# Performance work log

Hardware: AMD Instinct MI355X
Metric: run time of the kernel (lower is better)

The kernel has to match this reference:

```python
import math
import jax, jax.numpy as jnp
import numpy as np

B, S, D, H = 4, 2048, 768, 12
HD = D // H  # 64


def setup_inputs() -> dict:
    key = jax.random.key(0)
    ks = jax.random.split(key, 10)
    sc = 0.02
    return {
        "hidden_states": jax.random.normal(ks[0], (B, S, D), dtype=jnp.float32),
        "attention_mask": jax.random.randint(ks[1], (1, H, S, S), 0, 2).astype(jnp.bool_),
        "q_w": jax.random.normal(ks[2], (D, D), dtype=jnp.float32) * sc,
        "q_b": jax.random.normal(ks[3], (D,), dtype=jnp.float32) * sc,
        "k_w": jax.random.normal(ks[4], (D, D), dtype=jnp.float32) * sc,
        "k_b": jax.random.normal(ks[5], (D,), dtype=jnp.float32) * sc,
        "v_w": jax.random.normal(ks[6], (D, D), dtype=jnp.float32) * sc,
        "v_b": jax.random.normal(ks[7], (D,), dtype=jnp.float32) * sc,
        "out_w": jax.random.normal(ks[8], (D, D), dtype=jnp.float32) * sc,
        "out_b": jax.random.normal(ks[9], (D,), dtype=jnp.float32) * sc,
    }


def _split_heads(x):
    # [B, S, D] -> [B, H, S, HD]
    b, s, _ = x.shape
    return x.reshape(b, s, H, HD).transpose(0, 2, 1, 3)


def reference(hidden_states, attention_mask, q_w, q_b, k_w, k_b, v_w, v_b, out_w, out_b):
    q = _split_heads(hidden_states @ q_w.T + q_b)
    k = _split_heads(hidden_states @ k_w.T + k_b)
    v = _split_heads(hidden_states @ v_w.T + v_b)
    scores = jnp.einsum("bhqd,bhkd->bhqk", q, k) / math.sqrt(HD)
    # prune_mode, before softmax: masked_fill(~mask, -inf)
    scores = jnp.where(attention_mask, scores, -jnp.inf)
    probs = jax.nn.softmax(scores, axis=-1)  # [B, H, S, S]
    ctx = jnp.einsum("bhqk,bhkd->bhqd", probs, v)
    ctx = ctx.transpose(0, 2, 1, 3).reshape(hidden_states.shape[0], -1, D)
    return ctx @ out_w.T + out_b
```

## Files before the change

kernel.cpp:

```cpp
#include <hip/hip_runtime.h>
#include <hip/hip_bf16.h>

#define B_ 4
#define S_ 2048
#define D_ 768
#define H_ 12
#define HD_ 64

typedef __attribute__((ext_vector_type(8))) short bf16x8;
typedef __attribute__((ext_vector_type(4))) float floatx4;

#define QSCALE 0.18033688011112042f

__device__ __forceinline__ unsigned short f2bf(float x) {
    union { float f; unsigned int u; } v; v.f = x;
    unsigned int r = v.u + 0x7fffu + ((v.u >> 16) & 1u);
    return (unsigned short)(r >> 16);
}

__device__ __forceinline__ unsigned int pk2bf(float a, float b) {
    __hip_bfloat162 h = __float22bfloat162_rn(make_float2(a, b));
    unsigned int u;
    __builtin_memcpy(&u, &h, 4);
    return u;
}

__device__ __forceinline__ void gload_lds16(const void* g, void* l) {
    __builtin_amdgcn_global_load_lds(
        (const __attribute__((address_space(1))) unsigned int*)g,
        (__attribute__((address_space(3))) unsigned int*)l, 16, 0, 0);
}

__device__ __forceinline__ bf16x8 ld_b64x2(const unsigned short* p) {
    union { bf16x8 v; unsigned long long q[2]; } u;
    u.q[0] = *(const unsigned long long*)p;
    u.q[1] = *(const unsigned long long*)(p + 4);
    return u.v;
}

__global__ void cast_f32_bf16(const float* __restrict__ src,
                              unsigned short* __restrict__ dst, int n4) {
    int i = blockIdx.x * 256 + threadIdx.x;
    if (i >= n4) return;
    float4 f = ((const float4*)src)[i];
    ushort4 o;
    o.x = f2bf(f.x); o.y = f2bf(f.y); o.z = f2bf(f.z); o.w = f2bf(f.w);
    ((ushort4*)dst)[i] = o;
}

__global__ void cast_w4(const float* __restrict__ w0, const float* __restrict__ w1,
                        const float* __restrict__ w2, const float* __restrict__ w3,
                        unsigned short* __restrict__ dst, int n4 ) {
    const float* src = (blockIdx.y == 0) ? w0 : (blockIdx.y == 1) ? w1
                     : (blockIdx.y == 2) ? w2 : w3;
    unsigned short* d = dst + (size_t)blockIdx.y * (size_t)n4 * 4;
    int i = blockIdx.x * 256 + threadIdx.x;
    if (i >= n4) return;
    float4 f = ((const float4*)src)[i];
    ushort4 o;
    o.x = f2bf(f.x); o.y = f2bf(f.y); o.z = f2bf(f.z); o.w = f2bf(f.w);
    ((ushort4*)d)[i] = o;
}

__global__ void pack_mask(const int* __restrict__ mask,
                          unsigned long long* __restrict__ bits) {
    size_t gw = (size_t)(blockIdx.x * 256 + threadIdx.x) >> 6;
    int lane = threadIdx.x & 63;
    size_t base = gw * 256;
    unsigned long long b0 = __ballot(mask[base + lane] != 0);
    unsigned long long b1 = __ballot(mask[base + 64 + lane] != 0);
    unsigned long long b2 = __ballot(mask[base + 128 + lane] != 0);
    unsigned long long b3 = __ballot(mask[base + 192 + lane] != 0);
    if (lane == 0) {
        bits[gw * 4 + 0] = b0; bits[gw * 4 + 1] = b1;
        bits[gw * 4 + 2] = b2; bits[gw * 4 + 3] = b3;
    }
}

__global__ __launch_bounds__(256) void qkv_gemm(
    const unsigned short* __restrict__ Xb,
    const unsigned short* __restrict__ Wq, const unsigned short* __restrict__ Wk,
    const unsigned short* __restrict__ Wv,
    const float* __restrict__ bq, const float* __restrict__ bk,
    const float* __restrict__ bv,
    unsigned short* __restrict__ Qo, unsigned short* __restrict__ Ko,
    unsigned short* __restrict__ Vo)
{
    const int z = blockIdx.z;
    const unsigned short* W = (z == 0) ? Wq : (z == 1) ? Wk : Wv;
    const float* bias = (z == 0) ? bq : (z == 1) ? bk : bv;
    unsigned short* Out = (z == 0) ? Qo : (z == 1) ? Ko : Vo;
    const float scale = (z == 0) ? QSCALE : 1.0f;

    const int m0 = blockIdx.x * 128;
    const int n0 = blockIdx.y * 128;

    __shared__ alignas(16) unsigned short SM[8192];
    unsigned short* As = SM;
    unsigned short* Bs = SM + 4096;

    const int t = threadIdx.x;
    const int lane = t & 63, w = t >> 6;
    const int c = lane & 15, quad = lane >> 4;
    const int wm = (w & 1) * 64, wn = (w >> 1) * 64;

    floatx4 acc[4][4];
#pragma unroll
    for (int i = 0; i < 4; i++)
#pragma unroll
        for (int j = 0; j < 4; j++) acc[i][j] = (floatx4){0.f, 0.f, 0.f, 0.f};

    for (int k0 = 0; k0 < 768; k0 += 32) {
#pragma unroll
        for (int i = 0; i < 2; i++) {
            int chunk = i * 4 + w;
            int row = chunk * 16 + (lane >> 2);
            int c8 = (lane & 3) * 8;
            gload_lds16(&Xb[(size_t)(m0 + row) * 768 + k0 + c8], &As[chunk * 512]);
            gload_lds16(&W [(size_t)(n0 + row) * 768 + k0 + c8], &Bs[chunk * 512]);
        }
        __syncthreads();
        bf16x8 a[4], b[4];
#pragma unroll
        for (int i = 0; i < 4; i++)
            a[i] = *(const bf16x8*)&As[(wm + i * 16 + c) * 32 + quad * 8];
#pragma unroll
        for (int j = 0; j < 4; j++)
            b[j] = *(const bf16x8*)&Bs[(wn + j * 16 + c) * 32 + quad * 8];
#pragma unroll
        for (int i = 0; i < 4; i++)
#pragma unroll
            for (int j = 0; j < 4; j++)
                acc[i][j] = __builtin_amdgcn_mfma_f32_16x16x32_bf16(
                    a[i], b[j], acc[i][j], 0, 0, 0);
        __syncthreads();
    }

    if (z == 2) {
        const int bb = m0 >> 11, ssb = m0 & 2047;
#pragma unroll
        for (int half = 0; half < 2; half++) {
            if ((w >> 1) == half) {
#pragma unroll
                for (int j = 0; j < 4; j++) {
                    int n_l = j * 16 + c;
                    float bias_n = bias[n0 + half * 64 + n_l];
#pragma unroll
                    for (int i = 0; i < 4; i++) {
#pragma unroll
                        for (int r = 0; r < 4; r++) {
                            int m = wm + i * 16 + quad * 4 + r;
                            int ms = m ^ (c << 3);
                            SM[n_l * 128 + ms] = f2bf(acc[i][j][r] + bias_n);
                        }
                    }
                }
            }
            __syncthreads();
#pragma unroll
            for (int rb = 0; rb < 2; rb++) {
                int n_l = (t >> 3) + rb * 32;
                int ch = t & 7;
                int n_abs = n0 + half * 64 + n_l;
                int hh = n_abs >> 6, dd = n_abs & 63;
                unsigned short* dst =
                    Out + (((size_t)(bb * H_ + hh)) * 64 + dd) * S_ + ssb;
#pragma unroll
                for (int p = 0; p < 2; p++) {
                    int mc = ch + p * 8;
                    uint4 v = *(const uint4*)&SM[n_l * 128 + ((mc ^ (n_l & 15)) * 8)];
                    *(uint4*)&dst[mc * 8] = v;
                }
            }
            __syncthreads();
        }
    } else {
#pragma unroll
        for (int i = 0; i < 4; i++) {
#pragma unroll
            for (int j = 0; j < 4; j++) {
                int nn = n0 + wn + j * 16 + c;
                float bias_n = bias[nn];
                int hh = nn >> 6, dd = nn & 63;
#pragma unroll
                for (int r = 0; r < 4; r++) {
                    int mm = m0 + wm + i * 16 + quad * 4 + r;
                    int bb = mm >> 11, ss = mm & 2047;
                    float v = (acc[i][j][r] + bias_n) * scale;
                    Out[(((size_t)(bb * H_ + hh)) * S_ + ss) * 64 + dd] = f2bf(v);
                }
            }
        }
    }
}

__global__ __launch_bounds__(256) void out_gemm(
    const unsigned short* __restrict__ Cb, const unsigned short* __restrict__ Wo,
    const float* __restrict__ bo, float* __restrict__ out)
{
    const int m0 = blockIdx.x * 128;
    const int n0 = blockIdx.y * 128;

    __shared__ alignas(16) unsigned short As[128 * 32];
    __shared__ alignas(16) unsigned short Bs[128 * 32];

    const int t = threadIdx.x;
    const int lane = t & 63, w = t >> 6;
    const int c = lane & 15, quad = lane >> 4;
    const int wm = (w & 1) * 64, wn = (w >> 1) * 64;

    floatx4 acc[4][4];
#pragma unroll
    for (int i = 0; i < 4; i++)
#pragma unroll
        for (int j = 0; j < 4; j++) acc[i][j] = (floatx4){0.f, 0.f, 0.f, 0.f};

    for (int k0 = 0; k0 < 768; k0 += 32) {
#pragma unroll
        for (int i = 0; i < 2; i++) {
            int chunk = i * 4 + w;
            int row = chunk * 16 + (lane >> 2);
            int c8 = (lane & 3) * 8;
            gload_lds16(&Cb[(size_t)(m0 + row) * 768 + k0 + c8], &As[chunk * 512]);
            gload_lds16(&Wo[(size_t)(n0 + row) * 768 + k0 + c8], &Bs[chunk * 512]);
        }
        __syncthreads();
        bf16x8 a[4], b[4];
#pragma unroll
        for (int i = 0; i < 4; i++)
            a[i] = *(const bf16x8*)&As[(wm + i * 16 + c) * 32 + quad * 8];
#pragma unroll
        for (int j = 0; j < 4; j++)
            b[j] = *(const bf16x8*)&Bs[(wn + j * 16 + c) * 32 + quad * 8];
#pragma unroll
        for (int i = 0; i < 4; i++)
#pragma unroll
            for (int j = 0; j < 4; j++)
                acc[i][j] = __builtin_amdgcn_mfma_f32_16x16x32_bf16(
                    a[i], b[j], acc[i][j], 0, 0, 0);
        __syncthreads();
    }

#pragma unroll
    for (int i = 0; i < 4; i++) {
#pragma unroll
        for (int j = 0; j < 4; j++) {
            int nn = n0 + wn + j * 16 + c;
            float bias_n = bo[nn];
#pragma unroll
            for (int r = 0; r < 4; r++) {
                int mm = m0 + wm + i * 16 + quad * 4 + r;
                out[(size_t)mm * 768 + nn] = acc[i][j][r] + bias_n;
            }
        }
    }
}

__global__ __launch_bounds__(256) void attn(
    const unsigned short* __restrict__ Q, const unsigned short* __restrict__ K,
    const unsigned short* __restrict__ Vt,
    const unsigned long long* __restrict__ mbits,
    unsigned short* __restrict__ ctx)
{
    const int qt = blockIdx.x;
    const int bh = blockIdx.y;
    const int b = bh / H_, h = bh % H_;

    const unsigned short* Qp = Q + (size_t)bh * S_ * 64 + (size_t)qt * 64 * 64;
    const unsigned short* Kp = K + (size_t)bh * S_ * 64;
    const unsigned short* Vp = Vt + (size_t)bh * 64 * S_;

    __shared__ alignas(16) unsigned short Ks[2][64 * 64];
    __shared__ alignas(16) unsigned short Vs[2][64 * 64];
    __shared__ alignas(16) unsigned short Ps[4][16 * 68];

    const int t = threadIdx.x;
    const int lane = t & 63, w = t >> 6;
    const int c = lane & 15, quad = lane >> 4;

    bf16x8 aq0 = *(const bf16x8*)&Qp[(size_t)(w * 16 + c) * 64 + quad * 8];
    bf16x8 aq1 = *(const bf16x8*)&Qp[(size_t)(w * 16 + c) * 64 + 32 + quad * 8];

    const unsigned long long* mrow =
        mbits + ((size_t)h * S_ + qt * 64 + w * 16 + quad * 4) * (S_ / 64);

    floatx4 acc_o[4];
#pragma unroll
    for (int i = 0; i < 4; i++) acc_o[i] = (floatx4){0.f, 0.f, 0.f, 0.f};
    float lp[4] = {0.f, 0.f, 0.f, 0.f};

    const int srow = (lane >> 3);
    const int rc0 = ((quad     ) ^ (c & 7)) * 8;
    const int rc1 = ((quad + 4) ^ (c & 7)) * 8;

#pragma unroll
    for (int i = 0; i < 2; i++) {
        int chunk = i * 4 + w;
        int row = chunk * 8 + srow;
        int col8 = (((lane & 7) ^ ((row >> 2) & 7))) * 8;
        gload_lds16(&Kp[(size_t)row * 64 + col8], &Ks[0][chunk * 512]);
        gload_lds16(&Vp[(size_t)row * S_ + col8], &Vs[0][chunk * 512]);
    }

    for (int kt = 0; kt < S_ / 64; kt++) {
        const int cur = kt & 1;
        __syncthreads();
        if (kt + 1 < S_ / 64) {
#pragma unroll
            for (int i = 0; i < 2; i++) {
                int chunk = i * 4 + w;
                int row = chunk * 8 + srow;
                int col8 = (((lane & 7) ^ ((row >> 2) & 7))) * 8;
                gload_lds16(&Kp[(size_t)((kt + 1) * 64 + row) * 64 + col8],
                            &Ks[cur ^ 1][chunk * 512]);
                gload_lds16(&Vp[(size_t)row * S_ + (kt + 1) * 64 + col8],
                            &Vs[cur ^ 1][chunk * 512]);
            }
        }

        floatx4 sacc[4];
#pragma unroll
        for (int nt = 0; nt < 4; nt++) {
            int kr = 4 * c + nt;
            bf16x8 bk0 = *(const bf16x8*)&Ks[cur][kr * 64 + rc0];
            bf16x8 bk1 = *(const bf16x8*)&Ks[cur][kr * 64 + rc1];
            floatx4 zz = (floatx4){0.f, 0.f, 0.f, 0.f};
            zz = __builtin_amdgcn_mfma_f32_16x16x32_bf16(aq0, bk0, zz, 0, 0, 0);
            zz = __builtin_amdgcn_mfma_f32_16x16x32_bf16(aq1, bk1, zz, 0, 0, 0);
            sacc[nt] = zz;
        }

#pragma unroll
        for (int r = 0; r < 4; r++) {
            unsigned int nib = (unsigned int)(mrow[r * (S_ / 64) + kt] >> (4 * c)) & 15u;
            float p0 = (nib & 1u) ? __builtin_amdgcn_exp2f(sacc[0][r]) : 0.f;
            float p1 = (nib & 2u) ? __builtin_amdgcn_exp2f(sacc[1][r]) : 0.f;
            float p2 = (nib & 4u) ? __builtin_amdgcn_exp2f(sacc[2][r]) : 0.f;
            float p3 = (nib & 8u) ? __builtin_amdgcn_exp2f(sacc[3][r]) : 0.f;
            lp[r] += (p0 + p1) + (p2 + p3);
            unsigned long long pk =
                (unsigned long long)pk2bf(p0, p1) |
                ((unsigned long long)pk2bf(p2, p3) << 32);
            *(unsigned long long*)&Ps[w][(quad * 4 + r) * 68 + 4 * c] = pk;
        }
        asm volatile("" ::: "memory");

        bf16x8 ap0 = ld_b64x2(&Ps[w][c * 68 + quad * 8]);
        bf16x8 ap1 = ld_b64x2(&Ps[w][c * 68 + 32 + quad * 8]);
#pragma unroll
        for (int nt = 0; nt < 4; nt++) {
            int vr = 4 * c + nt;
            bf16x8 bv0 = *(const bf16x8*)&Vs[cur][vr * 64 + rc0];
            bf16x8 bv1 = *(const bf16x8*)&Vs[cur][vr * 64 + rc1];
            acc_o[nt] = __builtin_amdgcn_mfma_f32_16x16x32_bf16(ap0, bv0, acc_o[nt], 0, 0, 0);
            acc_o[nt] = __builtin_amdgcn_mfma_f32_16x16x32_bf16(ap1, bv1, acc_o[nt], 0, 0, 0);
        }
    }

#pragma unroll
    for (int r = 0; r < 4; r++) {
        float s = lp[r];
#pragma unroll
        for (int o = 1; o < 16; o <<= 1) s += __shfl_xor(s, o, 64);
        lp[r] = s;
    }

#pragma unroll
    for (int nt = 0; nt < 4; nt++) {
#pragma unroll
        for (int r = 0; r < 4; r++) {
            int qrow = qt * 64 + w * 16 + quad * 4 + r;
            int dd = 4 * c + nt;
            float v = acc_o[nt][r] / lp[r];
            ctx[((size_t)b * S_ + qrow) * 768 + h * 64 + dd] = f2bf(v);
        }
    }
}

extern "C" void kernel_launch(void* const* d_in, const int* in_sizes, int n_in,
                              void* d_out, int out_size, void* d_ws, size_t ws_size,
                              hipStream_t stream) {
    const float* hs    = (const float*)d_in[0];
    const int*   mask  = (const int*)d_in[1];
    const float* q_w   = (const float*)d_in[2];
    const float* q_b   = (const float*)d_in[3];
    const float* k_w   = (const float*)d_in[4];
    const float* k_b   = (const float*)d_in[5];
    const float* v_w   = (const float*)d_in[6];
    const float* v_b   = (const float*)d_in[7];
    const float* out_w = (const float*)d_in[8];
    const float* out_b = (const float*)d_in[9];
    float* out = (float*)d_out;

    unsigned short* Xb  = (unsigned short*)d_ws;
    unsigned short* Wqb = Xb + 6291456;
    unsigned short* Wkb = Wqb + 589824;
    unsigned short* Wvb = Wkb + 589824;
    unsigned short* Wob = Wvb + 589824;
    unsigned short* Qb  = Wob + 589824;
    unsigned short* Kb  = Qb + 6291456;
    unsigned short* Vtb = Kb + 6291456;
    unsigned short* Cb  = Vtb + 6291456;
    unsigned long long* mbits = (unsigned long long*)(Cb + 6291456);

    cast_f32_bf16<<<6144, 256, 0, stream>>>(hs, Xb, 1572864);
    cast_w4<<<dim3(576, 4), 256, 0, stream>>>(q_w, k_w, v_w, out_w, Wqb, 147456);
    pack_mask<<<49152, 256, 0, stream>>>(mask, mbits);
    qkv_gemm<<<dim3(64, 6, 3), 256, 0, stream>>>(Xb, Wqb, Wkb, Wvb,
                                                 q_b, k_b, v_b, Qb, Kb, Vtb);
    attn<<<dim3(32, 48), 256, 0, stream>>>(Qb, Kb, Vtb, mbits, Cb);
    out_gemm<<<dim3(64, 6), 256, 0, stream>>>(Cb, Wob, out_b, out);
}
```

Measured before the change: 508.1 us.

## Double attention query tile per block and stage GEMM epilogues through LDS

The attention kernel now processes 128 query rows per block, with each wave handling two 16-row subtiles. Each K/V tile loaded into shared memory is therefore reused across twice as many queries, halving K/V global traffic and the grid size. The Q/K epilogue of the QKV GEMM and the output GEMM epilogue now stage results through swizzled shared memory so global stores are coalesced 16-byte writes instead of scattered 2- or 4-byte ones. The trade-offs are fewer blocks (768), higher register pressure in attention, and extra barriers in the epilogues.

```diff
diff --git a/kernel.cpp b/kernel.cpp
--- a/kernel.cpp
+++ b/kernel.cpp
@@ -136,8 +136,8 @@
         __syncthreads();
     }
 
+    const int bb = m0 >> 11, ssb = m0 & 2047;
     if (z == 2) {
-        const int bb = m0 >> 11, ssb = m0 & 2047;
 #pragma unroll
         for (int half = 0; half < 2; half++) {
             if ((w >> 1) == half) {
@@ -176,20 +176,37 @@
         }
     } else {
 #pragma unroll
-        for (int i = 0; i < 4; i++) {
-#pragma unroll
-            for (int j = 0; j < 4; j++) {
-                int nn = n0 + wn + j * 16 + c;
-                float bias_n = bias[nn];
-                int hh = nn >> 6, dd = nn & 63;
-#pragma unroll
-                for (int r = 0; r < 4; r++) {
-                    int mm = m0 + wm + i * 16 + quad * 4 + r;
-                    int bb = mm >> 11, ss = mm & 2047;
-                    float v = (acc[i][j][r] + bias_n) * scale;
-                    Out[(((size_t)(bb * H_ + hh)) * S_ + ss) * 64 + dd] = f2bf(v);
+        for (int half = 0; half < 2; half++) {
+            if ((w >> 1) == half) {
+#pragma unroll
+                for (int j = 0; j < 4; j++) {
+                    float bias_n = bias[n0 + half * 64 + j * 16 + c];
+#pragma unroll
+                    for (int i = 0; i < 4; i++) {
+#pragma unroll
+                        for (int r = 0; r < 4; r++) {
+                            int m = wm + i * 16 + quad * 4 + r;
+                            int chunk = (j * 2 + (c >> 3)) ^ ((m >> 1) & 7);
+                            SM[m * 64 + chunk * 8 + (c & 7)] =
+                                f2bf((acc[i][j][r] + bias_n) * scale);
+                        }
+                    }
                 }
             }
+            __syncthreads();
+            {
+                int hh = (n0 >> 6) + half;
+                unsigned short* dst =
+                    Out + ((size_t)(bb * H_ + hh) * S_ + ssb) * 64;
+#pragma unroll
+                for (int i = 0; i < 4; i++) {
+                    int idx = i * 256 + t;
+                    int m = idx >> 3, ch = idx & 7;
+                    uint4 v = *(const uint4*)&SM[m * 64 + ((ch ^ ((m >> 1) & 7)) * 8)];
+                    *(uint4*)&dst[(size_t)m * 64 + ch * 8] = v;
+                }
+            }
+            __syncthreads();
         }
     }
 }
@@ -201,8 +218,9 @@
     const int m0 = blockIdx.x * 128;
     const int n0 = blockIdx.y * 128;
 
-    __shared__ alignas(16) unsigned short As[128 * 32];
-    __shared__ alignas(16) unsigned short Bs[128 * 32];
+    __shared__ alignas(16) unsigned short SM[8192];
+    unsigned short* As = SM;
+    unsigned short* Bs = SM + 4096;
 
     const int t = threadIdx.x;
     const int lane = t & 63, w = t >> 6;
@@ -241,18 +259,36 @@
         __syncthreads();
     }
 
-#pragma unroll
-    for (int i = 0; i < 4; i++) {
-#pragma unroll
-        for (int j = 0; j < 4; j++) {
-            int nn = n0 + wn + j * 16 + c;
-            float bias_n = bo[nn];
-#pragma unroll
-            for (int r = 0; r < 4; r++) {
-                int mm = m0 + wm + i * 16 + quad * 4 + r;
-                out[(size_t)mm * 768 + nn] = acc[i][j][r] + bias_n;
-            }
-        }
+    float* SMf = (float*)SM;
+#pragma unroll
+    for (int qtr = 0; qtr < 4; qtr++) {
+        if ((qtr >> 1) == (wn >> 6)) {
+            int j0 = (qtr & 1) * 2;
+#pragma unroll
+            for (int jj = 0; jj < 2; jj++) {
+                int j = j0 + jj;
+                float bias_n = bo[n0 + wn + j * 16 + c];
+                int chunk = jj * 4 + (c >> 2);
+#pragma unroll
+                for (int i = 0; i < 4; i++) {
+#pragma unroll
+                    for (int r = 0; r < 4; r++) {
+                        int m = wm + i * 16 + quad * 4 + r;
+                        SMf[m * 32 + ((chunk ^ (m & 7)) * 4) + (c & 3)] =
+                            acc[i][j][r] + bias_n;
+                    }
+                }
+            }
+        }
+        __syncthreads();
+#pragma unroll
+        for (int i = 0; i < 4; i++) {
+            int idx = i * 256 + t;
+            int m = idx >> 3, ch = idx & 7;
+            float4 v = *(const float4*)&SMf[m * 32 + ((ch ^ (m & 7)) * 4)];
+            *(float4*)&out[(size_t)(m0 + m) * 768 + n0 + qtr * 32 + ch * 4] = v;
+        }
+        __syncthreads();
     }
 }
 
@@ -266,7 +302,7 @@
     const int bh = blockIdx.y;
     const int b = bh / H_, h = bh % H_;
 
-    const unsigned short* Qp = Q + (size_t)bh * S_ * 64 + (size_t)qt * 64 * 64;
+    const unsigned short* Qp = Q + (size_t)bh * S_ * 64 + (size_t)qt * 128 * 64;
     const unsigned short* Kp = K + (size_t)bh * S_ * 64;
     const unsigned short* Vp = Vt + (size_t)bh * 64 * S_;
 
@@ -278,16 +314,22 @@
     const int lane = t & 63, w = t >> 6;
     const int c = lane & 15, quad = lane >> 4;
 
-    bf16x8 aq0 = *(const bf16x8*)&Qp[(size_t)(w * 16 + c) * 64 + quad * 8];
-    bf16x8 aq1 = *(const bf16x8*)&Qp[(size_t)(w * 16 + c) * 64 + 32 + quad * 8];
+    bf16x8 aq[2][2];
+#pragma unroll
+    for (int st = 0; st < 2; st++) {
+        aq[st][0] = *(const bf16x8*)&Qp[(size_t)(w * 32 + st * 16 + c) * 64 + quad * 8];
+        aq[st][1] = *(const bf16x8*)&Qp[(size_t)(w * 32 + st * 16 + c) * 64 + 32 + quad * 8];
+    }
 
     const unsigned long long* mrow =
-        mbits + ((size_t)h * S_ + qt * 64 + w * 16 + quad * 4) * (S_ / 64);
-
-    floatx4 acc_o[4];
-#pragma unroll
-    for (int i = 0; i < 4; i++) acc_o[i] = (floatx4){0.f, 0.f, 0.f, 0.f};
-    float lp[4] = {0.f, 0.f, 0.f, 0.f};
+        mbits + ((size_t)h * S_ + qt * 128 + w * 32 + quad * 4) * (S_ / 64);
+
+    floatx4 acc_o[2][4];
+#pragma unroll
+    for (int st = 0; st < 2; st++)
+#pragma unroll
+        for (int i = 0; i < 4; i++) acc_o[st][i] = (floatx4){0.f, 0.f, 0.f, 0.f};
+    float lp[2][4] = {{0.f, 0.f, 0.f, 0.f}, {0.f, 0.f, 0.f, 0.f}};
 
     const int srow = (lane >> 3);
     const int rc0 = ((quad     ) ^ (c & 7)) * 8;
@@ -318,63 +360,71 @@
             }
         }
 
-        floatx4 sacc[4];
-#pragma unroll
-        for (int nt = 0; nt < 4; nt++) {
-            int kr = 4 * c + nt;
-            bf16x8 bk0 = *(const bf16x8*)&Ks[cur][kr * 64 + rc0];
-            bf16x8 bk1 = *(const bf16x8*)&Ks[cur][kr * 64 + rc1];
-            floatx4 zz = (floatx4){0.f, 0.f, 0.f, 0.f};
-            zz = __builtin_amdgcn_mfma_f32_16x16x32_bf16(aq0, bk0, zz, 0, 0, 0);
-            zz = __builtin_amdgcn_mfma_f32_16x16x32_bf16(aq1, bk1, zz, 0, 0, 0);
-            sacc[nt] = zz;
-        }
-
+#pragma unroll
+        for (int st = 0; st < 2; st++) {
+            floatx4 sacc[4];
+#pragma unroll
+            for (int nt = 0; nt < 4; nt++) {
+                int kr = 4 * c + nt;
+                bf16x8 bk0 = *(const bf16x8*)&Ks[cur][kr * 64 + rc0];
+                bf16x8 bk1 = *(const bf16x8*)&Ks[cur][kr * 64 + rc1];
+                floatx4 zz = (floatx4){0.f, 0.f, 0.f, 0.f};
+                zz = __builtin_amdgcn_mfma_f32_16x16x32_bf16(aq[st][0], bk0, zz, 0, 0, 0);
+                zz = __builtin_amdgcn_mfma_f32_16x16x32_bf16(aq[st][1], bk1, zz, 0, 0, 0);
+                sacc[nt] = zz;
+            }
+
+            asm volatile("" ::: "memory");
+#pragma unroll
+            for (int r = 0; r < 4; r++) {
+                unsigned int nib =
+                    (unsigned int)(mrow[st * 16 * (S_ / 64) + r * (S_ / 64) + kt] >> (4 * c)) & 15u;
+                float p0 = (nib & 1u) ? __builtin_amdgcn_exp2f(sacc[0][r]) : 0.f;
+                float p1 = (nib & 2u) ? __builtin_amdgcn_exp2f(sacc[1][r]) : 0.f;
+                float p2 = (nib & 4u) ? __builtin_amdgcn_exp2f(sacc[2][r]) : 0.f;
+                float p3 = (nib & 8u) ? __builtin_amdgcn_exp2f(sacc[3][r]) : 0.f;
+                lp[st][r] += (p0 + p1) + (p2 + p3);
+                unsigned long long pk =
+                    (unsigned long long)pk2bf(p0, p1) |
+                    ((unsigned long long)pk2bf(p2, p3) << 32);
+                *(unsigned long long*)&Ps[w][(quad * 4 + r) * 68 + 4 * c] = pk;
+            }
+            asm volatile("" ::: "memory");
+
+            bf16x8 ap0 = ld_b64x2(&Ps[w][c * 68 + quad * 8]);
+            bf16x8 ap1 = ld_b64x2(&Ps[w][c * 68 + 32 + quad * 8]);
+#pragma unroll
+            for (int nt = 0; nt < 4; nt++) {
+                int vr = 4 * c + nt;
+                bf16x8 bv0 = *(const bf16x8*)&Vs[cur][vr * 64 + rc0];
+                bf16x8 bv1 = *(const bf16x8*)&Vs[cur][vr * 64 + rc1];
+                acc_o[st][nt] = __builtin_amdgcn_mfma_f32_16x16x32_bf16(ap0, bv0, acc_o[st][nt], 0, 0, 0);
+                acc_o[st][nt] = __builtin_amdgcn_mfma_f32_16x16x32_bf16(ap1, bv1, acc_o[st][nt], 0, 0, 0);
+            }
+        }
+    }
+
+#pragma unroll
+    for (int st = 0; st < 2; st++)
 #pragma unroll
         for (int r = 0; r < 4; r++) {
-            unsigned int nib = (unsigned int)(mrow[r * (S_ / 64) + kt] >> (4 * c)) & 15u;
-            float p0 = (nib & 1u) ? __builtin_amdgcn_exp2f(sacc[0][r]) : 0.f;
-            float p1 = (nib & 2u) ? __builtin_amdgcn_exp2f(sacc[1][r]) : 0.f;
-            float p2 = (nib & 4u) ? __builtin_amdgcn_exp2f(sacc[2][r]) : 0.f;
-            float p3 = (nib & 8u) ? __builtin_amdgcn_exp2f(sacc[3][r]) : 0.f;
-            lp[r] += (p0 + p1) + (p2 + p3);
-            unsigned long long pk =
-                (unsigned long long)pk2bf(p0, p1) |
-                ((unsigned long long)pk2bf(p2, p3) << 32);
-            *(unsigned long long*)&Ps[w][(quad * 4 + r) * 68 + 4 * c] = pk;
-        }
-        asm volatile("" ::: "memory");
-
-        bf16x8 ap0 = ld_b64x2(&Ps[w][c * 68 + quad * 8]);
-        bf16x8 ap1 = ld_b64x2(&Ps[w][c * 68 + 32 + quad * 8]);
-#pragma unroll
-        for (int nt = 0; nt < 4; nt++) {
-            int vr = 4 * c + nt;
-            bf16x8 bv0 = *(const bf16x8*)&Vs[cur][vr * 64 + rc0];
-            bf16x8 bv1 = *(const bf16x8*)&Vs[cur][vr * 64 + rc1];
-            acc_o[nt] = __builtin_amdgcn_mfma_f32_16x16x32_bf16(ap0, bv0, acc_o[nt], 0, 0, 0);
-            acc_o[nt] = __builtin_amdgcn_mfma_f32_16x16x32_bf16(ap1, bv1, acc_o[nt], 0, 0, 0);
-        }
-    }
-
-#pragma unroll
-    for (int r = 0; r < 4; r++) {
-        float s = lp[r];
-#pragma unroll
-        for (int o = 1; o < 16; o <<= 1) s += __shfl_xor(s, o, 64);
-        lp[r] = s;
-    }
-
-#pragma unroll
-    for (int nt = 0; nt < 4; nt++) {
-#pragma unroll
-        for (int r = 0; r < 4; r++) {
-            int qrow = qt * 64 + w * 16 + quad * 4 + r;
-            int dd = 4 * c + nt;
-            float v = acc_o[nt][r] / lp[r];
-            ctx[((size_t)b * S_ + qrow) * 768 + h * 64 + dd] = f2bf(v);
-        }
-    }
+            float s = lp[st][r];
+#pragma unroll
+            for (int o = 1; o < 16; o <<= 1) s += __shfl_xor(s, o, 64);
+            lp[st][r] = s;
+        }
+
+#pragma unroll
+    for (int st = 0; st < 2; st++)
+#pragma unroll
+        for (int nt = 0; nt < 4; nt++)
+#pragma unroll
+            for (int r = 0; r < 4; r++) {
+                int qrow = qt * 128 + w * 32 + st * 16 + quad * 4 + r;
+                int dd = 4 * c + nt;
+                float v = acc_o[st][nt][r] / lp[st][r];
+                ctx[((size_t)b * S_ + qrow) * 768 + h * 64 + dd] = f2bf(v);
+            }
 }
 
 extern "C" void kernel_launch(void* const* d_in, const int* in_sizes, int n_in,
@@ -408,6 +458,6 @@
     pack_mask<<<49152, 256, 0, stream>>>(mask, mbits);
     qkv_gemm<<<dim3(64, 6, 3), 256, 0, stream>>>(Xb, Wqb, Wkb, Wvb,
                                                  q_b, k_b, v_b, Qb, Kb, Vtb);
-    attn<<<dim3(32, 48), 256, 0, stream>>>(Qb, Kb, Vtb, mbits, Cb);
+    attn<<<dim3(16, 48), 256, 0, stream>>>(Qb, Kb, Vtb, mbits, Cb);
     out_gemm<<<dim3(64, 6), 256, 0, stream>>>(Cb, Wob, out_b, out);
 }
```

Result: no change. 500.0 us (-1.6%).
